# Performance work log

Measured on AMD Instinct MI355X. Metric: run time of the kernel, lower is better.

## Reference

```python
import jax, jax.numpy as jnp
import numpy as np

BATCH, IN_F, OUT_F = 8192, 4096, 4096


def setup_inputs() -> dict:
    key = jax.random.key(0)
    kx, kw = jax.random.split(key)
    x = jax.random.normal(kx, (BATCH, IN_F), dtype=jnp.float32)
    # weights binarized to {-1, +1} as in __init__ (uniform(-1,1) then sign)
    W = jnp.where(jax.random.normal(kw, (OUT_F, IN_F)) > 0, 1.0, -1.0).astype(jnp.float32)
    return {"x": x, "W": W}


def reference(x, W):
    # forward: input thresholded to {0,1} (x>0 -> 1, else 0), then x_bin @ W^T, no bias
    x_bin = (x > 0).astype(x.dtype)
    return jnp.matmul(x_bin, W.T)  # [batch, out_features]
```

## Files before the change

### kernel.cpp

```cpp
#include <hip/hip_runtime.h>
#include <stdint.h>

typedef __attribute__((ext_vector_type(4)))  int   v4i;
typedef __attribute__((ext_vector_type(8)))  int   v8i;
typedef __attribute__((ext_vector_type(16))) float v16f;

#define BATCH 8192
#define KDIM  4096
#define NOUT  4096
#define KB    (KDIM / 2)
#define BK_B  128
#define NT    (KDIM / 256)

__global__ __launch_bounds__(256) void pack_x4(const float* __restrict__ x,
                                               uint32_t* __restrict__ xb) {
    int t = blockIdx.x * 256 + threadIdx.x;
    const float4* p = (const float4*)x + (size_t)t * 2;
    float4 f0 = p[0];
    float4 f1 = p[1];
    uint32_t b = (f0.x > 0.f ? 0x2u        : 0u)
               | (f0.y > 0.f ? 0x20u       : 0u)
               | (f0.z > 0.f ? 0x200u      : 0u)
               | (f0.w > 0.f ? 0x2000u     : 0u)
               | (f1.x > 0.f ? 0x20000u    : 0u)
               | (f1.y > 0.f ? 0x200000u   : 0u)
               | (f1.z > 0.f ? 0x2000000u  : 0u)
               | (f1.w > 0.f ? 0x20000000u : 0u);
    xb[t] = b;
}

__global__ __launch_bounds__(256) void pack_w4(const float* __restrict__ w,
                                               uint32_t* __restrict__ wb) {
    int t = blockIdx.x * 256 + threadIdx.x;
    const float4* p = (const float4*)w + (size_t)t * 2;
    float4 f0 = p[0];
    float4 f1 = p[1];
    uint32_t b = (f0.x > 0.f ? 0x2u        : 0xAu)
               | (f0.y > 0.f ? 0x20u       : 0xA0u)
               | (f0.z > 0.f ? 0x200u      : 0xA00u)
               | (f0.w > 0.f ? 0x2000u     : 0xA000u)
               | (f1.x > 0.f ? 0x20000u    : 0xA0000u)
               | (f1.y > 0.f ? 0x200000u   : 0xA00000u)
               | (f1.z > 0.f ? 0x2000000u  : 0xA000000u)
               | (f1.w > 0.f ? 0x20000000u : 0xA0000000u);
    wb[t] = b;
}

__global__ __launch_bounds__(512, 2) void bin_gemm4(const uint8_t* __restrict__ A,
                                                    const uint8_t* __restrict__ B,
                                                    float* __restrict__ C) {
    __shared__ __align__(16) uint8_t sm[131072];

    const int tid  = threadIdx.x;
    const int w    = tid >> 6;
    const int lane = tid & 63;
    const int l31  = lane & 31;
    const int kc   = lane >> 5;
    const int rsw  = lane & 7;

    const int Mbase = blockIdx.y * 256;
    const int Nbase = blockIdx.x * 256;
    const int wm = (w >> 2) * 128;
    const int wn = (w & 3) * 64;

    const int srow = w * 8 + (lane >> 3);
    const int swz  = ((lane & 7) ^ ((lane >> 3) & 7)) * 16;

    const uint8_t* pA = A + (size_t)(Mbase + srow) * KB + swz;
    const uint8_t* pB = B + (size_t)(Nbase + srow) * KB + swz;
    const int ldsw = w * 1024;

    v16f acc[4][2] = {};

    #pragma unroll
    for (int L = 0; L < 4; ++L) {
        __builtin_amdgcn_global_load_lds(
            (__attribute__((address_space(1))) void*)(pA + (size_t)(L * 64) * KB),
            (__attribute__((address_space(3))) void*)(sm + L * 8192 + ldsw), 16, 0, 0);
        __builtin_amdgcn_global_load_lds(
            (__attribute__((address_space(1))) void*)(pB + (size_t)(L * 64) * KB),
            (__attribute__((address_space(3))) void*)(sm + 32768 + L * 8192 + ldsw), 16, 0, 0);
    }
    __syncthreads();

    for (int t = 0; t < NT; ++t) {
        if (t + 1 < NT) {
            const int nbuf = (t + 1) & 1;
            const int kof  = (t + 1) * BK_B;
            #pragma unroll
            for (int L = 0; L < 4; ++L) {
                __builtin_amdgcn_global_load_lds(
                    (__attribute__((address_space(1))) void*)(pA + (size_t)(L * 64) * KB + kof),
                    (__attribute__((address_space(3))) void*)(sm + nbuf * 65536 + L * 8192 + ldsw),
                    16, 0, 0);
                __builtin_amdgcn_global_load_lds(
                    (__attribute__((address_space(1))) void*)(pB + (size_t)(L * 64) * KB + kof),
                    (__attribute__((address_space(3))) void*)(sm + nbuf * 65536 + 32768 + L * 8192 + ldsw),
                    16, 0, 0);
            }
        }

        const uint8_t* sA = sm + (t & 1) * 65536;
        const uint8_t* sB = sA + 32768;

        #pragma unroll
        for (int ks = 0; ks < 4; ++ks) {
            v4i bf[2];
            #pragma unroll
            for (int nb = 0; nb < 2; ++nb)
                bf[nb] = *(const v4i*)(sB + (wn + nb * 32 + l31) * 128
                                       + ((ks * 2 + kc) ^ rsw) * 16);
            #pragma unroll
            for (int mb = 0; mb < 4; ++mb) {
                v4i af = *(const v4i*)(sA + (wm + mb * 32 + l31) * 128
                                       + ((ks * 2 + kc) ^ rsw) * 16);
                v8i a8 = {af[0], af[1], af[2], af[3], 0, 0, 0, 0};
                #pragma unroll
                for (int nb = 0; nb < 2; ++nb) {
                    v8i b8 = {bf[nb][0], bf[nb][1], bf[nb][2], bf[nb][3], 0, 0, 0, 0};
                    acc[mb][nb] = __builtin_amdgcn_mfma_scale_f32_32x32x64_f8f6f4(
                        a8, b8, acc[mb][nb], 4, 4,
                        0, 0x7F7F7F7F, 0, 0x7F7F7F7F);
                }
            }
        }

        __syncthreads();
    }

    float* Cp = C + (size_t)(Mbase + wm + 4 * kc) * NOUT + (Nbase + wn + l31);
    #pragma unroll
    for (int mb = 0; mb < 4; ++mb)
        #pragma unroll
        for (int nb = 0; nb < 2; ++nb)
            #pragma unroll
            for (int r = 0; r < 16; ++r)
                Cp[(size_t)(mb * 32 + (r & 3) + 8 * (r >> 2)) * NOUT + nb * 32]
                    = acc[mb][nb][r];
}

extern "C" void kernel_launch(void* const* d_in, const int* in_sizes, int n_in,
                              void* d_out, int out_size, void* d_ws, size_t ws_size,
                              hipStream_t stream) {
    const float* x = (const float*)d_in[0];
    const float* W = (const float*)d_in[1];
    float* out = (float*)d_out;

    uint8_t* xb = (uint8_t*)d_ws;
    uint8_t* wb = (uint8_t*)d_ws + (size_t)BATCH * KDIM / 2;

    pack_x4<<<(BATCH * (size_t)KDIM / 8) / 256, 256, 0, stream>>>(x, (uint32_t*)xb);
    pack_w4<<<((size_t)NOUT * KDIM / 8) / 256, 256, 0, stream>>>(W, (uint32_t*)wb);

    dim3 grid(NOUT / 256, BATCH / 256);
    bin_gemm4<<<grid, 512, 0, stream>>>(xb, wb, out);
}
```

Baseline: 324.5 us.

## Shrink GEMM block to 256x128 with 4 waves and single-buffered LDS

Block tile drops from 256x256 with 8 waves to 256x128 with 4 waves, and the grid doubles along N. Double buffering is removed in favour of a single 48KB LDS buffer that is loaded and then synced each K step. The goal is smaller LDS use so more blocks fit per CU for occupancy, in place of explicit prefetch. In exchange, load latency is no longer overlapped inside a block, and each fetched tile of X is reused across fewer output columns, so global traffic rises.

```diff
diff --git a/kernel.cpp b/kernel.cpp
--- a/kernel.cpp
+++ b/kernel.cpp
@@ -46,10 +46,10 @@
     wb[t] = b;
 }
 
-__global__ __launch_bounds__(512, 2) void bin_gemm4(const uint8_t* __restrict__ A,
+__global__ __launch_bounds__(256, 2) void bin_gemm4(const uint8_t* __restrict__ A,
                                                     const uint8_t* __restrict__ B,
                                                     float* __restrict__ C) {
-    __shared__ __align__(16) uint8_t sm[131072];
+    __shared__ __align__(16) uint8_t sm[49152];
 
     const int tid  = threadIdx.x;
     const int w    = tid >> 6;
@@ -59,61 +59,47 @@
     const int rsw  = lane & 7;
 
     const int Mbase = blockIdx.y * 256;
-    const int Nbase = blockIdx.x * 256;
-    const int wm = (w >> 2) * 128;
-    const int wn = (w & 3) * 64;
+    const int Nbase = blockIdx.x * 128;
+    const int wm = (w >> 1) * 128;
+    const int wn = (w & 1) * 64;
 
-    const int srow = w * 8 + (lane >> 3);
+    const int grow = lane >> 3;
     const int swz  = ((lane & 7) ^ ((lane >> 3) & 7)) * 16;
 
-    const uint8_t* pA = A + (size_t)(Mbase + srow) * KB + swz;
-    const uint8_t* pB = B + (size_t)(Nbase + srow) * KB + swz;
-    const int ldsw = w * 1024;
+    const uint8_t* pA = A + (size_t)(Mbase + w * 64 + grow) * KB + swz;
+    const uint8_t* pB = B + (size_t)(Nbase + w * 32 + grow) * KB + swz;
+    uint8_t* sA = sm;
+    uint8_t* sB = sm + 32768;
 
     v16f acc[4][2] = {};
 
-    #pragma unroll
-    for (int L = 0; L < 4; ++L) {
-        __builtin_amdgcn_global_load_lds(
-            (__attribute__((address_space(1))) void*)(pA + (size_t)(L * 64) * KB),
-            (__attribute__((address_space(3))) void*)(sm + L * 8192 + ldsw), 16, 0, 0);
-        __builtin_amdgcn_global_load_lds(
-            (__attribute__((address_space(1))) void*)(pB + (size_t)(L * 64) * KB),
-            (__attribute__((address_space(3))) void*)(sm + 32768 + L * 8192 + ldsw), 16, 0, 0);
-    }
-    __syncthreads();
+    for (int t = 0; t < NT; ++t) {
+        const int kof = t * BK_B;
 
-    for (int t = 0; t < NT; ++t) {
-        if (t + 1 < NT) {
-            const int nbuf = (t + 1) & 1;
-            const int kof  = (t + 1) * BK_B;
-            #pragma unroll
-            for (int L = 0; L < 4; ++L) {
-                __builtin_amdgcn_global_load_lds(
-                    (__attribute__((address_space(1))) void*)(pA + (size_t)(L * 64) * KB + kof),
-                    (__attribute__((address_space(3))) void*)(sm + nbuf * 65536 + L * 8192 + ldsw),
-                    16, 0, 0);
-                __builtin_amdgcn_global_load_lds(
-                    (__attribute__((address_space(1))) void*)(pB + (size_t)(L * 64) * KB + kof),
-                    (__attribute__((address_space(3))) void*)(sm + nbuf * 65536 + 32768 + L * 8192 + ldsw),
-                    16, 0, 0);
-            }
-        }
-
-        const uint8_t* sA = sm + (t & 1) * 65536;
-        const uint8_t* sB = sA + 32768;
+        #pragma unroll
+        for (int L = 0; L < 8; ++L)
+            __builtin_amdgcn_global_load_lds(
+                (__attribute__((address_space(1))) void*)(pA + (size_t)(L * 8) * KB + kof),
+                (__attribute__((address_space(3))) void*)(sA + (w * 64 + L * 8) * 128),
+                16, 0, 0);
+        #pragma unroll
+        for (int L = 0; L < 4; ++L)
+            __builtin_amdgcn_global_load_lds(
+                (__attribute__((address_space(1))) void*)(pB + (size_t)(L * 8) * KB + kof),
+                (__attribute__((address_space(3))) void*)(sB + (w * 32 + L * 8) * 128),
+                16, 0, 0);
+        __syncthreads();
 
         #pragma unroll
         for (int ks = 0; ks < 4; ++ks) {
+            const int slot = ((ks * 2 + kc) ^ rsw) * 16;
             v4i bf[2];
             #pragma unroll
             for (int nb = 0; nb < 2; ++nb)
-                bf[nb] = *(const v4i*)(sB + (wn + nb * 32 + l31) * 128
-                                       + ((ks * 2 + kc) ^ rsw) * 16);
+                bf[nb] = *(const v4i*)(sB + (wn + nb * 32 + l31) * 128 + slot);
             #pragma unroll
             for (int mb = 0; mb < 4; ++mb) {
-                v4i af = *(const v4i*)(sA + (wm + mb * 32 + l31) * 128
-                                       + ((ks * 2 + kc) ^ rsw) * 16);
+                v4i af = *(const v4i*)(sA + (wm + mb * 32 + l31) * 128 + slot);
                 v8i a8 = {af[0], af[1], af[2], af[3], 0, 0, 0, 0};
                 #pragma unroll
                 for (int nb = 0; nb < 2; ++nb) {
@@ -124,7 +110,6 @@
                 }
             }
         }
-
         __syncthreads();
     }
 
@@ -152,6 +137,6 @@
     pack_x4<<<(BATCH * (size_t)KDIM / 8) / 256, 256, 0, stream>>>(x, (uint32_t*)xb);
     pack_w4<<<((size_t)NOUT * KDIM / 8) / 256, 256, 0, stream>>>(W, (uint32_t*)wb);
 
-    dim3 grid(NOUT / 256, BATCH / 256);
-    bin_gemm4<<<grid, 512, 0, stream>>>(xb, wb, out);
+    dim3 grid(NOUT / 128, BATCH / 256);
+    bin_gemm4<<<grid, 256, 0, stream>>>(xb, wb, out);
 }
```

Measured after the change: 330.2 us. No clear change (+1.8%).
